# Optimization experiments

Hardware: AMD Instinct MI355X
Metric: run time of the kernel (lower is better)

Reference implementation:

```python
import jax, jax.numpy as jnp
import numpy as np

U, I, D, E, B = 100000, 50000, 128, 3200000, 4096
KEEP_PROB = 0.8

def setup_inputs() -> dict:
    key = jax.random.key(0)
    ks = jax.random.split(key, 9)
    return {
        "user_emb": 0.01 * jax.random.normal(ks[0], (U, D), dtype=jnp.float32),
        "item_emb": 0.01 * jax.random.normal(ks[1], (I, D), dtype=jnp.float32),
        "vals": jax.random.uniform(ks[2], (E,), dtype=jnp.float32),
        "keep_mask": jax.random.uniform(ks[3], (E,), dtype=jnp.float32),
        "rows": jax.random.randint(ks[4], (E,), 0, U, dtype=jnp.int32),
        "cols": jax.random.randint(ks[5], (E,), 0, I, dtype=jnp.int32),
        "user": jax.random.randint(ks[6], (B,), 0, U, dtype=jnp.int32),
        "pos_item": jax.random.randint(ks[7], (B,), 0, I, dtype=jnp.int32),
        "neg_item": jax.random.randint(ks[8], (B,), 0, I, dtype=jnp.int32),
    }

def reference(user_emb, item_emb, vals, keep_mask, rows, cols, user, pos_item, neg_item):
    # Edge dropout: keep edge iff uniform < keep_prob, rescale by 1/keep_prob.
    # (Equivalent to torch's index filtering, expressed as zeroed values.)
    dvals = jnp.where(keep_mask < KEEP_PROB, vals / KEEP_PROB, 0.0)
    u0, i0 = user_emb, item_emb
    # i_1 = spmm(A^T, u_0): scatter edge messages by item (col) index.  [I, D]
    i1 = jax.ops.segment_sum(dvals[:, None] * u0[rows], cols, num_segments=item_emb.shape[0])
    # u_1 = spmm(A, i_0): scatter edge messages by user (row) index.    [U, D]
    u1 = jax.ops.segment_sum(dvals[:, None] * i0[cols], rows, num_segments=user_emb.shape[0])
    # Layer combination (mean of layer-0 and layer-1), gathered per batch.
    u = (u0[user] + u1[user]) * 0.5        # [B, D]
    i = (i0[pos_item] + i1[pos_item]) * 0.5
    j = (i0[neg_item] + i1[neg_item]) * 0.5
    pos_score = jnp.sum(u * i, axis=1, keepdims=True)  # [B, 1]
    neg_score = jnp.sum(u * j, axis=1, keepdims=True)  # [B, 1]
    return (pos_score, neg_score)
```

## Files before the change

### kernel.cpp

```cpp
#include <hip/hip_runtime.h>

#define DIM 128
#define KEEP_PROB 0.8f
#define UCAP 96
#define ICAP 160
#define SMASK_WORDS 5120

__global__ void slot_kernel(const int* __restrict__ user, const int* __restrict__ pos,
                            const int* __restrict__ neg, int* __restrict__ u_slot,
                            int* __restrict__ i_slot, unsigned* __restrict__ u_mask,
                            unsigned* __restrict__ i_mask, int B) {
    int t = blockIdx.x * blockDim.x + threadIdx.x;
    if (t < B) {
        int u = user[t];
        u_slot[u] = t;
        atomicOr(&u_mask[u >> 5], 1u << (u & 31));
    } else if (t < 2 * B) {
        int it = pos[t - B];
        i_slot[it] = t - B;
        atomicOr(&i_mask[it >> 5], 1u << (it & 31));
    } else if (t < 3 * B) {
        int it = neg[t - 2 * B];
        i_slot[it] = (t - 2 * B) + B;
        atomicOr(&i_mask[it >> 5], 1u << (it & 31));
    }
}

template <bool LDS>
__global__ void fill_bucket_kernel(const float* __restrict__ vals, const float* __restrict__ keep,
                                   const int* __restrict__ rows, const int* __restrict__ cols,
                                   const int* __restrict__ u_slot, const int* __restrict__ i_slot,
                                   const unsigned* __restrict__ masks, int umw, int mw_total,
                                   int* __restrict__ cursor, int2* __restrict__ entries,
                                   int E, int B) {
    __shared__ unsigned sm[LDS ? SMASK_WORDS : 1];
    const unsigned *um, *im;
    if constexpr (LDS) {
        for (int i = threadIdx.x; i < mw_total; i += blockDim.x) sm[i] = masks[i];
        __syncthreads();
        um = sm; im = sm + umw;
    } else {
        um = masks; im = masks + umw;
    }

    int t = blockIdx.x * blockDim.x + threadIdx.x;
    int base = t * 8;
    if (base >= E) return;
    long long ib = (long long)B * UCAP;
    if (base + 7 < E) {
        float4 ka = *(const float4*)(keep + base), kb = *(const float4*)(keep + base + 4);
        float4 va = *(const float4*)(vals + base), vb = *(const float4*)(vals + base + 4);
        int4 ra = *(const int4*)(rows + base), rb = *(const int4*)(rows + base + 4);
        int4 ca = *(const int4*)(cols + base), cb = *(const int4*)(cols + base + 4);
        float kk[8] = {ka.x, ka.y, ka.z, ka.w, kb.x, kb.y, kb.z, kb.w};
        float vv[8] = {va.x, va.y, va.z, va.w, vb.x, vb.y, vb.z, vb.w};
        int rr[8] = {ra.x, ra.y, ra.z, ra.w, rb.x, rb.y, rb.z, rb.w};
        int cc[8] = {ca.x, ca.y, ca.z, ca.w, cb.x, cb.y, cb.z, cb.w};
#pragma unroll
        for (int j = 0; j < 8; j++) {
            if (kk[j] < KEEP_PROB) {
                int r = rr[j], c = cc[j];
                float dv = vv[j] * 1.25f;
                if ((um[r >> 5] >> (r & 31)) & 1u) {
                    int us = u_slot[r];
                    int p = atomicAdd(&cursor[us], 1);
                    if (p < UCAP) entries[(long long)us * UCAP + p] = make_int2(c, __float_as_int(dv));
                }
                if ((im[c >> 5] >> (c & 31)) & 1u) {
                    int is = i_slot[c];
                    int p = atomicAdd(&cursor[B + is], 1);
                    if (p < ICAP) entries[ib + (long long)is * ICAP + p] = make_int2(r, __float_as_int(dv));
                }
            }
        }
    } else {
        for (int e = base; e < E; e++) {
            if (keep[e] < KEEP_PROB) {
                int r = rows[e], c = cols[e];
                float dv = vals[e] * 1.25f;
                if ((um[r >> 5] >> (r & 31)) & 1u) {
                    int us = u_slot[r];
                    int p = atomicAdd(&cursor[us], 1);
                    if (p < UCAP) entries[(long long)us * UCAP + p] = make_int2(c, __float_as_int(dv));
                }
                if ((im[c >> 5] >> (c & 31)) & 1u) {
                    int is = i_slot[c];
                    int p = atomicAdd(&cursor[B + is], 1);
                    if (p < ICAP) entries[ib + (long long)is * ICAP + p] = make_int2(r, __float_as_int(dv));
                }
            }
        }
    }
}

__global__ void count_kernel(const float* __restrict__ keep, const int* __restrict__ rows,
                             const int* __restrict__ cols, const int* __restrict__ u_slot,
                             const int* __restrict__ i_slot, int* __restrict__ cnt,
                             int E, int B) {
    int t = blockIdx.x * blockDim.x + threadIdx.x;
    int base = t * 4;
    if (base >= E) return;
    for (int e = base; e < base + 4 && e < E; e++) {
        if (keep[e] < KEEP_PROB) {
            int us = u_slot[rows[e]];
            if (us >= 0) atomicAdd(&cnt[us], 1);
            int is = i_slot[cols[e]];
            if (is >= 0) atomicAdd(&cnt[B + is], 1);
        }
    }
}

__global__ void scan_kernel(const int* __restrict__ cnt, int* __restrict__ offs,
                            int* __restrict__ cursor, int n) {
    __shared__ int wave_tot[16];
    __shared__ int carry_s;
    int tid = threadIdx.x, lane = tid & 63, wv = tid >> 6;
    if (tid == 0) carry_s = 0;
    __syncthreads();
    for (int base = 0; base < n; base += 1024) {
        int v = (base + tid < n) ? cnt[base + tid] : 0;
        int x = v;
#pragma unroll
        for (int off = 1; off < 64; off <<= 1) {
            int y = __shfl_up(x, off);
            if (lane >= off) x += y;
        }
        if (lane == 63) wave_tot[wv] = x;
        __syncthreads();
        if (wv == 0 && lane < 16) {
            int tot = wave_tot[lane];
            int s = tot;
#pragma unroll
            for (int off = 1; off < 16; off <<= 1) {
                int y = __shfl_up(s, off);
                if (lane >= off) s += y;
            }
            wave_tot[lane] = s - tot;
        }
        __syncthreads();
        int excl = (x - v) + wave_tot[wv] + carry_s;
        if (base + tid < n) { offs[base + tid] = excl; cursor[base + tid] = excl; }
        __syncthreads();
        if (tid == 1023) carry_s += wave_tot[15] + x;
        __syncthreads();
    }
}

__global__ void fill_csr_kernel(const float* __restrict__ vals, const float* __restrict__ keep,
                                const int* __restrict__ rows, const int* __restrict__ cols,
                                const int* __restrict__ u_slot, const int* __restrict__ i_slot,
                                int* __restrict__ cursor, int2* __restrict__ entries,
                                long long cap, int E, int B) {
    int t = blockIdx.x * blockDim.x + threadIdx.x;
    int base = t * 4;
    if (base >= E) return;
    for (int e = base; e < base + 4 && e < E; e++) {
        if (keep[e] < KEEP_PROB) {
            float dv = vals[e] * 1.25f;
            int us = u_slot[rows[e]];
            if (us >= 0) {
                int p = atomicAdd(&cursor[us], 1);
                if (p < cap) entries[p] = make_int2(cols[e], __float_as_int(dv));
            }
            int is = i_slot[cols[e]];
            if (is >= 0) {
                int p = atomicAdd(&cursor[B + is], 1);
                if (p < cap) entries[p] = make_int2(rows[e], __float_as_int(dv));
            }
        }
    }
}

__global__ void gather_kernel(const int2* __restrict__ entries, const int* __restrict__ offs,
                              const int* __restrict__ cntp, const float* __restrict__ u0,
                              const float* __restrict__ i0, float* __restrict__ u1c,
                              float* __restrict__ i1c, int B, int mode, long long cap) {
    __shared__ float part[3][DIM];
    int wv = threadIdx.x >> 6;
    int lane = threadIdx.x & 63;
    int dest = blockIdx.x;

    const float* table;
    float* dst;
    if (dest < B) { table = i0; dst = u1c + (size_t)dest * DIM; }
    else          { table = u0; dst = i1c + (size_t)(dest - B) * DIM; }

    int n = cntp[dest];
    long long base;
    if (mode == 1) {
        if (dest < B) { base = (long long)dest * UCAP; if (n > UCAP) n = UCAP; }
        else { base = (long long)B * UCAP + (long long)(dest - B) * ICAP; if (n > ICAP) n = ICAP; }
    } else {
        base = offs[dest];
        if (base + (long long)n > cap) { long long rem = cap - base; n = rem < 0 ? 0 : (int)rem; }
    }

    int m = (n - wv + 3) >> 2;
    if (m < 0) m = 0;
    int o = lane * 2;
    float ax = 0.f, ay = 0.f;
    for (int k0 = 0; k0 < m; k0 += 64) {
        int my = k0 + lane;
        int2 e = make_int2(0, 0);
        if (my < m) e = entries[base + wv + 4 * (long long)my];
        int mm = m - k0;
        if (mm > 64) mm = 64;
        int j = 0;
        for (; j + 4 <= mm; j += 4) {
            int s0 = __shfl(e.x, j + 0), s1 = __shfl(e.x, j + 1);
            int s2 = __shfl(e.x, j + 2), s3 = __shfl(e.x, j + 3);
            float d0 = __int_as_float(__shfl(e.y, j + 0));
            float d1 = __int_as_float(__shfl(e.y, j + 1));
            float d2 = __int_as_float(__shfl(e.y, j + 2));
            float d3 = __int_as_float(__shfl(e.y, j + 3));
            float2 r0 = *(const float2*)(table + (size_t)s0 * DIM + o);
            float2 r1 = *(const float2*)(table + (size_t)s1 * DIM + o);
            float2 r2 = *(const float2*)(table + (size_t)s2 * DIM + o);
            float2 r3 = *(const float2*)(table + (size_t)s3 * DIM + o);
            ax += d0 * r0.x; ay += d0 * r0.y;
            ax += d1 * r1.x; ay += d1 * r1.y;
            ax += d2 * r2.x; ay += d2 * r2.y;
            ax += d3 * r3.x; ay += d3 * r3.y;
        }
        for (; j < mm; j++) {
            int s = __shfl(e.x, j);
            float dv = __int_as_float(__shfl(e.y, j));
            float2 r = *(const float2*)(table + (size_t)s * DIM + o);
            ax += dv * r.x; ay += dv * r.y;
        }
    }
    if (wv > 0) { part[wv - 1][o] = ax; part[wv - 1][o + 1] = ay; }
    __syncthreads();
    if (wv == 0) {
        ax += part[0][o] + part[1][o] + part[2][o];
        ay += part[0][o + 1] + part[1][o + 1] + part[2][o + 1];
        *(float2*)(dst + o) = make_float2(ax, ay);
    }
}

__global__ void score_kernel(const float* __restrict__ u0, const float* __restrict__ i0,
                             const float* __restrict__ u1c, const float* __restrict__ i1c,
                             const int* __restrict__ user, const int* __restrict__ pos,
                             const int* __restrict__ neg, const int* __restrict__ u_slot,
                             const int* __restrict__ i_slot, float* __restrict__ out, int B) {
    int wave = (blockIdx.x * blockDim.x + threadIdx.x) >> 6;
    int lane = threadIdx.x & 63;
    if (wave >= B) return;

    int ub = user[wave], pb = pos[wave], nb = neg[wave];
    int usl = u_slot[ub], psl = i_slot[pb], nsl = i_slot[nb];
    int o = lane * 2;

    float2 a0 = *(const float2*)(u0  + (size_t)ub  * DIM + o);
    float2 a1 = *(const float2*)(u1c + (size_t)usl * DIM + o);
    float2 p0 = *(const float2*)(i0  + (size_t)pb  * DIM + o);
    float2 p1 = *(const float2*)(i1c + (size_t)psl * DIM + o);
    float2 n0 = *(const float2*)(i0  + (size_t)nb  * DIM + o);
    float2 n1 = *(const float2*)(i1c + (size_t)nsl * DIM + o);

    float ux = (a0.x + a1.x) * 0.5f, uy = (a0.y + a1.y) * 0.5f;
    float px = (p0.x + p1.x) * 0.5f, py = (p0.y + p1.y) * 0.5f;
    float nx = (n0.x + n1.x) * 0.5f, ny = (n0.y + n1.y) * 0.5f;

    float ps = ux * px + uy * py;
    float ns = ux * nx + uy * ny;
    for (int off = 32; off > 0; off >>= 1) {
        ps += __shfl_down(ps, off);
        ns += __shfl_down(ns, off);
    }
    if (lane == 0) {
        out[wave]     = ps;
        out[B + wave] = ns;
    }
}

extern "C" void kernel_launch(void* const* d_in, const int* in_sizes, int n_in,
                              void* d_out, int out_size, void* d_ws, size_t ws_size,
                              hipStream_t stream) {
    const float* user_emb = (const float*)d_in[0];
    const float* item_emb = (const float*)d_in[1];
    const float* vals     = (const float*)d_in[2];
    const float* keep     = (const float*)d_in[3];
    const int*   rows     = (const int*)d_in[4];
    const int*   cols     = (const int*)d_in[5];
    const int*   user     = (const int*)d_in[6];
    const int*   pos      = (const int*)d_in[7];
    const int*   neg      = (const int*)d_in[8];
    float* out = (float*)d_out;

    int U = in_sizes[0] / DIM;
    int I = in_sizes[1] / DIM;
    int E = in_sizes[2];
    int B = in_sizes[6];

    int umw = ((U + 31) / 32 + 3) & ~3;
    int imw = ((I + 31) / 32 + 3) & ~3;

    char* p = (char*)d_ws;
    int* u_slot = (int*)p;              p += (size_t)U * 4;
    int* i_slot = (int*)p;              p += (size_t)I * 4;
    unsigned* u_mask = (unsigned*)p;    p += (size_t)umw * 4;
    unsigned* i_mask = (unsigned*)p;    p += (size_t)imw * 4;
    int* cnt    = (int*)p;              p += (size_t)3 * B * 4;
    int* offs   = (int*)p;              p += (size_t)3 * B * 4;
    int* cursor = (int*)p;              p += (size_t)3 * B * 4;
    float* u1c  = (float*)p;            p += (size_t)B * DIM * 4;
    float* i1c  = (float*)p;            p += (size_t)2 * B * DIM * 4;
    int2* entries = (int2*)p;
    size_t used = (size_t)(p - (char*)d_ws);
    long long avail = (long long)ws_size - (long long)used;

    long long bucket_entries = (long long)B * UCAP + (long long)2 * B * ICAP;
    int mode = (avail >= bucket_entries * (long long)sizeof(int2)) ? 1 : 0;

    hipMemsetAsync(u_mask, 0x00, (size_t)(umw + imw + 9 * B) * 4, stream);
    if (mode == 0) hipMemsetAsync(u_slot, 0xFF, (size_t)(U + I) * 4, stream);

    slot_kernel<<<(3 * B + 255) / 256, 256, 0, stream>>>(user, pos, neg, u_slot, i_slot,
                                                         u_mask, i_mask, B);

    long long cap;
    if (mode == 1) {
        cap = bucket_entries;
        int fb = ((E + 7) / 8 + 255) / 256;
        if (umw + imw <= SMASK_WORDS) {
            fill_bucket_kernel<true><<<fb, 256, 0, stream>>>(vals, keep, rows, cols, u_slot,
                                                             i_slot, u_mask, umw, umw + imw,
                                                             cursor, entries, E, B);
        } else {
            fill_bucket_kernel<false><<<fb, 256, 0, stream>>>(vals, keep, rows, cols, u_slot,
                                                              i_slot, u_mask, umw, umw + imw,
                                                              cursor, entries, E, B);
        }
        gather_kernel<<<3 * B, 256, 0, stream>>>(entries, offs, cursor, user_emb, item_emb,
                                                 u1c, i1c, B, 1, cap);
    } else {
        cap = avail / (long long)sizeof(int2);
        if (cap < 0) cap = 0;
        int cb = ((E + 3) / 4 + 255) / 256;
        count_kernel<<<cb, 256, 0, stream>>>(keep, rows, cols, u_slot, i_slot, cnt, E, B);
        scan_kernel<<<1, 1024, 0, stream>>>(cnt, offs, cursor, 3 * B);
        fill_csr_kernel<<<cb, 256, 0, stream>>>(vals, keep, rows, cols, u_slot, i_slot,
                                                cursor, entries, cap, E, B);
        gather_kernel<<<3 * B, 256, 0, stream>>>(entries, offs, cnt, user_emb, item_emb,
                                                 u1c, i1c, B, 0, cap);
    }

    score_kernel<<<(B * 64 + 255) / 256, 256, 0, stream>>>(user_emb, item_emb, u1c, i1c,
                                                           user, pos, neg, u_slot, i_slot,
                                                           out, B);
}
```

Before: 220.5 us.

## Fuse slot, bucket-fill, gather and score stages into one cooperative kernel

After: 825.3 us. +274.2%, slower.

```diff
diff --git a/kernel.cpp b/kernel.cpp
--- a/kernel.cpp
+++ b/kernel.cpp
@@ -1,10 +1,207 @@
 #include <hip/hip_runtime.h>
+#include <hip/hip_cooperative_groups.h>
+
+namespace cg = cooperative_groups;
 
 #define DIM 128
 #define KEEP_PROB 0.8f
 #define UCAP 96
 #define ICAP 160
 #define SMASK_WORDS 5120
+#define FGRID 1536
+
+__global__ __launch_bounds__(256, 6)
+void fused_kernel(const float* __restrict__ user_emb, const float* __restrict__ item_emb,
+                  const float* __restrict__ vals, const float* __restrict__ keep,
+                  const int* __restrict__ rows, const int* __restrict__ cols,
+                  const int* __restrict__ user, const int* __restrict__ pos,
+                  const int* __restrict__ neg,
+                  int* __restrict__ u_slot, int* __restrict__ i_slot,
+                  unsigned* __restrict__ u_mask,
+                  int* __restrict__ cursor, int2* __restrict__ entries,
+                  float* __restrict__ u1c, float* __restrict__ i1c,
+                  float* __restrict__ out,
+                  int E, int B, int umw, int mw_total) {
+    __shared__ unsigned sm[SMASK_WORDS];
+    cg::grid_group grid = cg::this_grid();
+    const int tid = threadIdx.x;
+    const int gtid = blockIdx.x * blockDim.x + tid;
+    const int gstride = gridDim.x * blockDim.x;
+
+    for (int i = gtid; i < mw_total; i += gstride) u_mask[i] = 0u;
+    for (int i = gtid; i < 3 * B; i += gstride) cursor[i] = 0;
+    grid.sync();
+
+    unsigned* i_mask = u_mask + umw;
+    for (int t = gtid; t < 3 * B; t += gstride) {
+        if (t < B) {
+            int u = user[t];
+            u_slot[u] = t;
+            atomicOr(&u_mask[u >> 5], 1u << (u & 31));
+        } else if (t < 2 * B) {
+            int it = pos[t - B];
+            i_slot[it] = t - B;
+            atomicOr(&i_mask[it >> 5], 1u << (it & 31));
+        } else {
+            int it = neg[t - 2 * B];
+            i_slot[it] = (t - 2 * B) + B;
+            atomicOr(&i_mask[it >> 5], 1u << (it & 31));
+        }
+    }
+    grid.sync();
+
+    {
+        for (int i = tid; i < mw_total; i += blockDim.x) sm[i] = u_mask[i];
+        __syncthreads();
+        const unsigned* um = sm;
+        const unsigned* im = sm + umw;
+        long long ib = (long long)B * UCAP;
+        int nchunk = (E + 7) >> 3;
+        for (int t = gtid; t < nchunk; t += gstride) {
+            int base = t * 8;
+            if (base + 7 < E) {
+                float4 ka = *(const float4*)(keep + base), kb = *(const float4*)(keep + base + 4);
+                float4 va = *(const float4*)(vals + base), vb = *(const float4*)(vals + base + 4);
+                int4 ra = *(const int4*)(rows + base), rb = *(const int4*)(rows + base + 4);
+                int4 ca = *(const int4*)(cols + base), cb = *(const int4*)(cols + base + 4);
+                float kk[8] = {ka.x, ka.y, ka.z, ka.w, kb.x, kb.y, kb.z, kb.w};
+                float vv[8] = {va.x, va.y, va.z, va.w, vb.x, vb.y, vb.z, vb.w};
+                int rr[8] = {ra.x, ra.y, ra.z, ra.w, rb.x, rb.y, rb.z, rb.w};
+                int cc[8] = {ca.x, ca.y, ca.z, ca.w, cb.x, cb.y, cb.z, cb.w};
+#pragma unroll
+                for (int j = 0; j < 8; j++) {
+                    if (kk[j] < KEEP_PROB) {
+                        int r = rr[j], c = cc[j];
+                        float dv = vv[j] * 1.25f;
+                        if ((um[r >> 5] >> (r & 31)) & 1u) {
+                            int us = u_slot[r];
+                            int p = atomicAdd(&cursor[us], 1);
+                            if (p < UCAP) entries[(long long)us * UCAP + p] = make_int2(c, __float_as_int(dv));
+                        }
+                        if ((im[c >> 5] >> (c & 31)) & 1u) {
+                            int is = i_slot[c];
+                            int p = atomicAdd(&cursor[B + is], 1);
+                            if (p < ICAP) entries[ib + (long long)is * ICAP + p] = make_int2(r, __float_as_int(dv));
+                        }
+                    }
+                }
+            } else {
+                for (int e = base; e < E; e++) {
+                    if (keep[e] < KEEP_PROB) {
+                        int r = rows[e], c = cols[e];
+                        float dv = vals[e] * 1.25f;
+                        if ((um[r >> 5] >> (r & 31)) & 1u) {
+                            int us = u_slot[r];
+                            int p = atomicAdd(&cursor[us], 1);
+                            if (p < UCAP) entries[(long long)us * UCAP + p] = make_int2(c, __float_as_int(dv));
+                        }
+                        if ((im[c >> 5] >> (c & 31)) & 1u) {
+                            int is = i_slot[c];
+                            int p = atomicAdd(&cursor[B + is], 1);
+                            if (p < ICAP) entries[ib + (long long)is * ICAP + p] = make_int2(r, __float_as_int(dv));
+                        }
+                    }
+                }
+            }
+        }
+    }
+    grid.sync();
+
+    {
+        float* part = (float*)sm;
+        int wv = tid >> 6;
+        int lane = tid & 63;
+        int o = lane * 2;
+        for (int dest = blockIdx.x; dest < 3 * B; dest += gridDim.x) {
+            const float* table;
+            float* dst;
+            long long base;
+            int n = cursor[dest];
+            if (dest < B) {
+                table = item_emb; dst = u1c + (size_t)dest * DIM;
+                base = (long long)dest * UCAP; if (n > UCAP) n = UCAP;
+            } else {
+                table = user_emb; dst = i1c + (size_t)(dest - B) * DIM;
+                base = (long long)B * UCAP + (long long)(dest - B) * ICAP;
+                if (n > ICAP) n = ICAP;
+            }
+            int m = (n - wv + 3) >> 2;
+            if (m < 0) m = 0;
+            float ax = 0.f, ay = 0.f;
+            for (int k0 = 0; k0 < m; k0 += 64) {
+                int my = k0 + lane;
+                int2 e = make_int2(0, 0);
+                if (my < m) e = entries[base + wv + 4 * (long long)my];
+                int mm = m - k0;
+                if (mm > 64) mm = 64;
+                int j = 0;
+                for (; j + 4 <= mm; j += 4) {
+                    int s0 = __shfl(e.x, j + 0), s1 = __shfl(e.x, j + 1);
+                    int s2 = __shfl(e.x, j + 2), s3 = __shfl(e.x, j + 3);
+                    float d0 = __int_as_float(__shfl(e.y, j + 0));
+                    float d1 = __int_as_float(__shfl(e.y, j + 1));
+                    float d2 = __int_as_float(__shfl(e.y, j + 2));
+                    float d3 = __int_as_float(__shfl(e.y, j + 3));
+                    float2 r0 = *(const float2*)(table + (size_t)s0 * DIM + o);
+                    float2 r1 = *(const float2*)(table + (size_t)s1 * DIM + o);
+                    float2 r2 = *(const float2*)(table + (size_t)s2 * DIM + o);
+                    float2 r3 = *(const float2*)(table + (size_t)s3 * DIM + o);
+                    ax += d0 * r0.x; ay += d0 * r0.y;
+                    ax += d1 * r1.x; ay += d1 * r1.y;
+                    ax += d2 * r2.x; ay += d2 * r2.y;
+                    ax += d3 * r3.x; ay += d3 * r3.y;
+                }
+                for (; j < mm; j++) {
+                    int s = __shfl(e.x, j);
+                    float dv = __int_as_float(__shfl(e.y, j));
+                    float2 r = *(const float2*)(table + (size_t)s * DIM + o);
+                    ax += dv * r.x; ay += dv * r.y;
+                }
+            }
+            if (wv > 0) { part[(wv - 1) * DIM + o] = ax; part[(wv - 1) * DIM + o + 1] = ay; }
+            __syncthreads();
+            if (wv == 0) {
+                ax += part[0 * DIM + o] + part[1 * DIM + o] + part[2 * DIM + o];
+                ay += part[0 * DIM + o + 1] + part[1 * DIM + o + 1] + part[2 * DIM + o + 1];
+                *(float2*)(dst + o) = make_float2(ax, ay);
+            }
+            __syncthreads();
+        }
+    }
+    grid.sync();
+
+    {
+        int lane = tid & 63;
+        int wstride = gstride >> 6;
+        for (int w = gtid >> 6; w < B; w += wstride) {
+            int ub = user[w], pb = pos[w], nb = neg[w];
+            int usl = u_slot[ub], psl = i_slot[pb], nsl = i_slot[nb];
+            int o = lane * 2;
+
+            float2 a0 = *(const float2*)(user_emb + (size_t)ub  * DIM + o);
+            float2 a1 = *(const float2*)(u1c      + (size_t)usl * DIM + o);
+            float2 p0 = *(const float2*)(item_emb + (size_t)pb  * DIM + o);
+            float2 p1 = *(const float2*)(i1c      + (size_t)psl * DIM + o);
+            float2 n0 = *(const float2*)(item_emb + (size_t)nb  * DIM + o);
+            float2 n1 = *(const float2*)(i1c      + (size_t)nsl * DIM + o);
+
+            float ux = (a0.x + a1.x) * 0.5f, uy = (a0.y + a1.y) * 0.5f;
+            float px = (p0.x + p1.x) * 0.5f, py = (p0.y + p1.y) * 0.5f;
+            float nx = (n0.x + n1.x) * 0.5f, ny = (n0.y + n1.y) * 0.5f;
+
+            float ps = ux * px + uy * py;
+            float ns = ux * nx + uy * ny;
+            for (int off = 32; off > 0; off >>= 1) {
+                ps += __shfl_down(ps, off);
+                ns += __shfl_down(ns, off);
+            }
+            if (lane == 0) {
+                out[w]     = ps;
+                out[B + w] = ns;
+            }
+        }
+    }
+}
 
 __global__ void slot_kernel(const int* __restrict__ user, const int* __restrict__ pos,
                             const int* __restrict__ neg, int* __restrict__ u_slot,
@@ -295,6 +492,7 @@
 
     int umw = ((U + 31) / 32 + 3) & ~3;
     int imw = ((I + 31) / 32 + 3) & ~3;
+    int mw_total = umw + imw;
 
     char* p = (char*)d_ws;
     int* u_slot = (int*)p;              p += (size_t)U * 4;
@@ -313,6 +511,20 @@
     long long bucket_entries = (long long)B * UCAP + (long long)2 * B * ICAP;
     int mode = (avail >= bucket_entries * (long long)sizeof(int2)) ? 1 : 0;
 
+    if (mode == 1 && mw_total <= SMASK_WORDS) {
+        void* args[] = {
+            (void*)&user_emb, (void*)&item_emb, (void*)&vals, (void*)&keep,
+            (void*)&rows, (void*)&cols, (void*)&user, (void*)&pos, (void*)&neg,
+            (void*)&u_slot, (void*)&i_slot, (void*)&u_mask,
+            (void*)&cursor, (void*)&entries, (void*)&u1c, (void*)&i1c,
+            (void*)&out, (void*)&E, (void*)&B, (void*)&umw, (void*)&mw_total
+        };
+        hipError_t err = hipLaunchCooperativeKernel((void*)fused_kernel, dim3(FGRID),
+                                                    dim3(256), args, 0, stream);
+        if (err == hipSuccess) return;
+        (void)hipGetLastError();
+    }
+
     hipMemsetAsync(u_mask, 0x00, (size_t)(umw + imw + 9 * B) * 4, stream);
     if (mode == 0) hipMemsetAsync(u_slot, 0xFF, (size_t)(U + I) * 4, stream);
 
@@ -323,13 +535,13 @@
     if (mode == 1) {
         cap = bucket_entries;
         int fb = ((E + 7) / 8 + 255) / 256;
-        if (umw + imw <= SMASK_WORDS) {
+        if (mw_total <= SMASK_WORDS) {
             fill_bucket_kernel<true><<<fb, 256, 0, stream>>>(vals, keep, rows, cols, u_slot,
-                                                             i_slot, u_mask, umw, umw + imw,
+                                                             i_slot, u_mask, umw, mw_total,
                                                              cursor, entries, E, B);
         } else {
             fill_bucket_kernel<false><<<fb, 256, 0, stream>>>(vals, keep, rows, cols, u_slot,
-                                                              i_slot, u_mask, umw, umw + imw,
+                                                              i_slot, u_mask, umw, mw_total,
                                                               cursor, entries, E, B);
         }
         gather_kernel<<<3 * B, 256, 0, stream>>>(entries, offs, cursor, user_emb, item_emb,
```
